# Performance work log

Hardware: AMD Instinct MI355X
Metric: run time of the kernel (lower is better)

Reference implementation:

```python
import jax, jax.numpy as jnp
import numpy as np

B, C, H, W = 8, 512, 64, 64
CQ = C // 8


def conv1x1(x, w, b):
    # x: [B,C,H,W], w: [O,C], b: [O] -> [B,O,H,W]
    return jnp.einsum('bchw,oc->bohw', x, w) + b[None, :, None, None]


def setup_inputs() -> dict:
    key = jax.random.key(0)
    ks = jax.random.split(key, 9)
    sc = 0.05
    return {
        'x2': jax.random.normal(ks[0], (B, C, H, W), jnp.float32),
        'x1': jax.random.normal(ks[1], (B, C, H, W), jnp.float32),
        'q_w': jax.random.normal(ks[2], (CQ, C), jnp.float32) * sc,
        'q_b': jax.random.normal(ks[3], (CQ,), jnp.float32) * sc,
        'k_w': jax.random.normal(ks[4], (CQ, C), jnp.float32) * sc,
        'k_b': jax.random.normal(ks[5], (CQ,), jnp.float32) * sc,
        'v_w': jax.random.normal(ks[6], (C, C), jnp.float32) * sc,
        'v_b': jax.random.normal(ks[7], (C,), jnp.float32) * sc,
        'gamma': jax.random.normal(ks[8], (1,), jnp.float32) * sc,
    }


def reference(x2, x1, q_w, q_b, k_w, k_b, v_w, v_b, gamma):
    h = x2.shape[2]
    q = conv1x1(x2, q_w, q_b)   # [B,CQ,H,W]
    k = conv1x1(x2, k_w, k_b)   # [B,CQ,H,W]
    v2 = conv1x1(x2, v_w, v_b)  # [B,C,H,W]
    v1 = conv1x1(x1, v_w, v_b)  # [B,C,H,W]

    # column (H) attention scores: query at (h,w) vs keys in same column
    energy_H = jnp.einsum('bchw,bcHw->bhwH', q, k)   # [B,H,W,H]
    # row (W) attention scores: query at (h,w) vs keys in same row
    energy_W = jnp.einsum('bchw,bchW->bhwW', q, k)   # [B,H,W,W]
    # NOTE: this module variant does NOT add the diagonal -inf mask.
    concate = jax.nn.softmax(jnp.concatenate([energy_H, energy_W], axis=3), axis=3)
    att_H = concate[..., :h]    # [B,H,W,H]
    att_W = concate[..., h:]    # [B,H,W,W]

    out_H2 = jnp.einsum('bcHw,bhwH->bchw', v2, att_H)
    out_W2 = jnp.einsum('bchW,bhwW->bchw', v2, att_W)
    out_H1 = jnp.einsum('bcHw,bhwH->bchw', v1, att_H)
    out_W1 = jnp.einsum('bchW,bhwW->bchw', v1, att_W)

    g = gamma[0]
    y2 = g * (out_H2 + out_W2) + x2
    y1 = g * (out_H1 + out_W1) + x1
    return (y2, y1)
```

## Files before the change

### kernel.cpp

```cpp
#include <hip/hip_runtime.h>
#include <cstdint>
#include <cstddef>

using u16 = unsigned short;
using u32 = unsigned int;

#define DI __device__ __forceinline__

typedef __attribute__((ext_vector_type(8))) short bf16x8;
typedef __attribute__((ext_vector_type(4))) float f32x4;

DI float bfu2f(u16 u) { return __uint_as_float(((u32)u) << 16); }
DI u16 f2bu(float f) {
    u32 x = __float_as_uint(f);
    return (u16)((x + 0x7fffu + ((x >> 16) & 1u)) >> 16);
}
DI u32 pk2(float a, float b) { return (u32)f2bu(a) | ((u32)f2bu(b) << 16); }

constexpr int CIN = 512;
constexpr int HW  = 4096;
constexpr size_t PLANE = 16777216ull;

__global__ __launch_bounds__(256) void proj_mfma(
    const float* __restrict__ x2, const float* __restrict__ x1,
    const float* __restrict__ q_w, const float* __restrict__ q_b,
    const float* __restrict__ k_w, const float* __restrict__ k_b,
    const float* __restrict__ v_w, const float* __restrict__ v_b,
    u16* __restrict__ oq, u16* __restrict__ ok,
    u16* __restrict__ ov2, u16* __restrict__ ov1)
{
    __shared__ u16 Wlds[128][40];
    __shared__ u16 Xlds[128][40];
    const int tid = threadIdx.x;
    const int m0  = blockIdx.y * 128;
    const int n0g = blockIdx.x * 128;
    const int b    = n0g >> 12;
    const int col0 = n0g & 4095;
    const float* Xb = ((m0 < 640) ? x2 : x1) + (size_t)b * CIN * HW;

    const bool isX = tid < 128;
    const int sr = tid & 127;
    const int mrow = m0 + sr;
    const float* wr;
    if (mrow < 64)        wr = q_w + (size_t)mrow * CIN;
    else if (mrow < 128)  wr = k_w + (size_t)(mrow - 64) * CIN;
    else if (mrow < 640)  wr = v_w + (size_t)(mrow - 128) * CIN;
    else                  wr = v_w + (size_t)(mrow - 640) * CIN;

    const int lane = tid & 63, wv = tid >> 6;
    const int wn = (wv & 1) * 64;
    const int wm = (wv >> 1) * 64;
    const int lr = lane & 15, lq = lane >> 4;

    f32x4 acc[4][4] = {};
    for (int kt = 0; kt < CIN; kt += 32) {
        if (isX) {
            const float* px = Xb + (size_t)kt * HW + col0 + sr;
            u32 pkv[16];
            #pragma unroll
            for (int kk = 0; kk < 16; kk++) {
                float a = px[(size_t)(2 * kk) * HW];
                float c = px[(size_t)(2 * kk + 1) * HW];
                pkv[kk] = pk2(a, c);
            }
            *(uint4*)&Xlds[sr][0]  = *(uint4*)&pkv[0];
            *(uint4*)&Xlds[sr][8]  = *(uint4*)&pkv[4];
            *(uint4*)&Xlds[sr][16] = *(uint4*)&pkv[8];
            *(uint4*)&Xlds[sr][24] = *(uint4*)&pkv[12];
        } else {
            const float* p = wr + kt;
            u32 pw[16];
            #pragma unroll
            for (int t = 0; t < 8; t++) {
                float4 f = *(const float4*)(p + 4 * t);
                pw[2 * t]     = pk2(f.x, f.y);
                pw[2 * t + 1] = pk2(f.z, f.w);
            }
            *(uint4*)&Wlds[sr][0]  = *(uint4*)&pw[0];
            *(uint4*)&Wlds[sr][8]  = *(uint4*)&pw[4];
            *(uint4*)&Wlds[sr][16] = *(uint4*)&pw[8];
            *(uint4*)&Wlds[sr][24] = *(uint4*)&pw[12];
        }
        __syncthreads();
        bf16x8 a[4], bb[4];
        #pragma unroll
        for (int i = 0; i < 4; i++)
            a[i] = *(const bf16x8*)&Xlds[wn + i * 16 + lr][lq * 8];
        #pragma unroll
        for (int j = 0; j < 4; j++)
            bb[j] = *(const bf16x8*)&Wlds[wm + j * 16 + lr][lq * 8];
        #pragma unroll
        for (int j = 0; j < 4; j++)
            #pragma unroll
            for (int i = 0; i < 4; i++)
                acc[i][j] = __builtin_amdgcn_mfma_f32_16x16x32_bf16(a[i], bb[j], acc[i][j], 0, 0, 0);
        __syncthreads();
    }
    #pragma unroll
    for (int j = 0; j < 4; j++) {
        const int mbase = m0 + wm + j * 16;
        const float* bp; u16* op; int ch0, cc;
        if (mbase < 64)       { bp = q_b; op = oq;  ch0 = mbase;       cc = 64;  }
        else if (mbase < 128) { bp = k_b; op = ok;  ch0 = mbase - 64;  cc = 64;  }
        else if (mbase < 640) { bp = v_b; op = ov2; ch0 = mbase - 128; cc = 512; }
        else                  { bp = v_b; op = ov1; ch0 = mbase - 640; cc = 512; }
        const int ch = ch0 + lr;
        const float bias = bp[ch];
        u16* obase = op + ((size_t)b * cc + ch) * HW + col0 + wn + lq * 4;
        #pragma unroll
        for (int i = 0; i < 4; i++) {
            uint2 pkd = { pk2(acc[i][j][0] + bias, acc[i][j][1] + bias),
                          pk2(acc[i][j][2] + bias, acc[i][j][3] + bias) };
            *(uint2*)(obase + i * 16) = pkd;
        }
    }
}

__global__ __launch_bounds__(256) void transpose64_bb(
    const u16* __restrict__ src, u16* __restrict__ dst)
{
    __shared__ u16 t[64][65];
    const size_t s = blockIdx.x;
    const u16* sp = src + s * 4096;
    u16* dp = dst + s * 4096;
    const int tid = threadIdx.x;
    #pragma unroll
    for (int i = 0; i < 16; i++) { int idx = tid + 256 * i; t[idx >> 6][idx & 63] = sp[idx]; }
    __syncthreads();
    #pragma unroll
    for (int i = 0; i < 16; i++) { int idx = tid + 256 * i; dp[idx] = t[idx & 63][idx >> 6]; }
}

__global__ __launch_bounds__(256) void transpose64_bb_inplace(u16* __restrict__ d)
{
    __shared__ u16 t[64][65];
    u16* p = d + (size_t)blockIdx.x * 4096;
    const int tid = threadIdx.x;
    #pragma unroll
    for (int i = 0; i < 16; i++) { int idx = tid + 256 * i; t[idx >> 6][idx & 63] = p[idx]; }
    __syncthreads();
    #pragma unroll
    for (int i = 0; i < 16; i++) { int idx = tid + 256 * i; p[idx] = t[idx & 63][idx >> 6]; }
}

__global__ __launch_bounds__(256) void transpose_cl(
    const u16* __restrict__ src, u16* __restrict__ dst)
{
    __shared__ u16 t[64][65];
    const int s = blockIdx.x;
    const int batch = s >> 6, tile = s & 63;
    const u16* sp = src + (size_t)batch * 262144 + (size_t)tile * 64;
    u16* dp = dst + (size_t)batch * 262144 + (size_t)tile * 4096;
    const int tid = threadIdx.x;
    {
        const int c = tid >> 2, x0 = (tid & 3) * 16;
        *(uint4*)&t[c][x0]     = *(const uint4*)(sp + (size_t)c * 4096 + x0);
        *(uint4*)&t[c][x0 + 8] = *(const uint4*)(sp + (size_t)c * 4096 + x0 + 8);
    }
    __syncthreads();
    {
        const int x = tid >> 2, c0 = (tid & 3) * 16;
        u16 tmp[16];
        #pragma unroll
        for (int i = 0; i < 16; i++) tmp[i] = t[c0 + i][x];
        *(uint4*)&dp[(size_t)x * 64 + c0]     = *(uint4*)&tmp[0];
        *(uint4*)&dp[(size_t)x * 64 + c0 + 8] = *(uint4*)&tmp[8];
    }
}

__global__ __launch_bounds__(256) void energy_h_mfma(
    const u16* __restrict__ qc, const u16* __restrict__ kc, float* __restrict__ e)
{
    __shared__ u16 Qs[64][72], Ks[64][72];
    const int w = blockIdx.x, b = blockIdx.y;
    const int tid = threadIdx.x;
    {
        const int row = tid >> 2, ch = (tid & 3) * 16;
        const size_t g = ((size_t)b * 4096 + (size_t)row * 64 + w) * 64 + ch;
        *(uint4*)&Qs[row][ch]     = *(const uint4*)(qc + g);
        *(uint4*)&Qs[row][ch + 8] = *(const uint4*)(qc + g + 8);
        *(uint4*)&Ks[row][ch]     = *(const uint4*)(kc + g);
        *(uint4*)&Ks[row][ch + 8] = *(const uint4*)(kc + g + 8);
    }
    __syncthreads();
    const int lane = tid & 63, wv = tid >> 6;
    const int mH = (wv & 1) * 32, nh = (wv >> 1) * 32;
    const int lr = lane & 15, lq = lane >> 4;
    f32x4 acc[2][2] = {};
    #pragma unroll
    for (int kt = 0; kt < 2; kt++) {
        const int k0 = kt * 32 + lq * 8;
        bf16x8 afr[2], bfr[2];
        #pragma unroll
        for (int i = 0; i < 2; i++) afr[i] = *(const bf16x8*)&Ks[mH + i * 16 + lr][k0];
        #pragma unroll
        for (int j = 0; j < 2; j++) bfr[j] = *(const bf16x8*)&Qs[nh + j * 16 + lr][k0];
        #pragma unroll
        for (int j = 0; j < 2; j++)
            #pragma unroll
            for (int i = 0; i < 2; i++)
                acc[i][j] = __builtin_amdgcn_mfma_f32_16x16x32_bf16(afr[i], bfr[j], acc[i][j], 0, 0, 0);
    }
    #pragma unroll
    for (int i = 0; i < 2; i++)
        #pragma unroll
        for (int j = 0; j < 2; j++) {
            const int h = nh + j * 16 + lr;
            const int Hp = mH + i * 16 + lq * 4;
            float4 v = make_float4(acc[i][j][0], acc[i][j][1], acc[i][j][2], acc[i][j][3]);
            *reinterpret_cast<float4*>(e + ((size_t)(b * 64 + h) * 64 + w) * 128 + Hp) = v;
        }
}

__global__ __launch_bounds__(256) void energy_w_mfma(
    const u16* __restrict__ qc, const u16* __restrict__ kc, float* __restrict__ e)
{
    __shared__ u16 Qs[64][72], Ks[64][72];
    const int h = blockIdx.x, b = blockIdx.y;
    const int tid = threadIdx.x;
    {
        const int row = tid >> 2, ch = (tid & 3) * 16;
        const size_t g = ((size_t)b * 4096 + (size_t)h * 64 + row) * 64 + ch;
        *(uint4*)&Qs[row][ch]     = *(const uint4*)(qc + g);
        *(uint4*)&Qs[row][ch + 8] = *(const uint4*)(qc + g + 8);
        *(uint4*)&Ks[row][ch]     = *(const uint4*)(kc + g);
        *(uint4*)&Ks[row][ch + 8] = *(const uint4*)(kc + g + 8);
    }
    __syncthreads();
    const int lane = tid & 63, wv = tid >> 6;
    const int mW = (wv & 1) * 32, nw = (wv >> 1) * 32;
    const int lr = lane & 15, lq = lane >> 4;
    f32x4 acc[2][2] = {};
    #pragma unroll
    for (int kt = 0; kt < 2; kt++) {
        const int k0 = kt * 32 + lq * 8;
        bf16x8 afr[2], bfr[2];
        #pragma unroll
        for (int i = 0; i < 2; i++) afr[i] = *(const bf16x8*)&Ks[mW + i * 16 + lr][k0];
        #pragma unroll
        for (int j = 0; j < 2; j++) bfr[j] = *(const bf16x8*)&Qs[nw + j * 16 + lr][k0];
        #pragma unroll
        for (int j = 0; j < 2; j++)
            #pragma unroll
            for (int i = 0; i < 2; i++)
                acc[i][j] = __builtin_amdgcn_mfma_f32_16x16x32_bf16(afr[i], bfr[j], acc[i][j], 0, 0, 0);
    }
    #pragma unroll
    for (int i = 0; i < 2; i++)
        #pragma unroll
        for (int j = 0; j < 2; j++) {
            const int w = nw + j * 16 + lr;
            const int Wp = mW + i * 16 + lq * 4;
            float4 v = make_float4(acc[i][j][0], acc[i][j][1], acc[i][j][2], acc[i][j][3]);
            *reinterpret_cast<float4*>(e + ((size_t)(b * 64 + h) * 64 + w) * 128 + 64 + Wp) = v;
        }
}

__global__ __launch_bounds__(256) void softmax128_bf(
    const float* __restrict__ e, u16* __restrict__ attb)
{
    const int pos = blockIdx.x * 4 + (threadIdx.x >> 6);
    const int l = threadIdx.x & 63;
    const float* p = e + (size_t)pos * 128;
    float v0 = p[l], v1 = p[l + 64];
    float m = fmaxf(v0, v1);
    #pragma unroll
    for (int o = 32; o > 0; o >>= 1) m = fmaxf(m, __shfl_xor(m, o, 64));
    float e0 = __expf(v0 - m), e1 = __expf(v1 - m);
    float s = e0 + e1;
    #pragma unroll
    for (int o = 32; o > 0; o >>= 1) s += __shfl_xor(s, o, 64);
    float inv = 1.0f / s;
    u16* q = attb + (size_t)pos * 128;
    q[l] = f2bu(e0 * inv);
    q[l + 64] = f2bu(e1 * inv);
}

__global__ __launch_bounds__(256) void agg_h_mfma(
    const u16* __restrict__ vTa, const u16* __restrict__ vTb,
    const u16* __restrict__ attb, u16* __restrict__ Pa, u16* __restrict__ Pb)
{
    __shared__ u16 Vs[128][72];
    __shared__ u16 As[64][72];
    const int mt = blockIdx.x, w = blockIdx.y, b = blockIdx.z;
    const u16* vT = (mt < 4) ? vTa : vTb;
    u16*       P  = (mt < 4) ? Pa  : Pb;
    const int c0 = (mt & 3) * 128;
    const int tid = threadIdx.x;
    const u16* va = vT + ((size_t)(b * 512 + c0) * 64 + w) * 64;
    const u16* ab = attb + ((size_t)b * 4096 + w) * 128;
    {
        const int r = tid >> 3, cB = (tid & 7) * 8;
        #pragma unroll
        for (int i = 0; i < 4; i++)
            *(uint4*)&Vs[r + 32 * i][cB] = *(const uint4*)(va + (size_t)(r + 32 * i) * 4096 + cB);
        #pragma unroll
        for (int i = 0; i < 2; i++)
            *(uint4*)&As[r + 32 * i][cB] = *(const uint4*)(ab + (size_t)(r + 32 * i) * 8192 + cB);
    }
    __syncthreads();
    const int lane = tid & 63, wv = tid >> 6;
    const int wm = (wv & 1) * 64, wn = (wv >> 1) * 32;
    const int lr = lane & 15, lq = lane >> 4;
    f32x4 acc[4][2] = {};
    #pragma unroll
    for (int kt = 0; kt < 2; kt++) {
        const int k0 = kt * 32 + lq * 8;
        bf16x8 afr[4], bfr[2];
        #pragma unroll
        for (int i = 0; i < 4; i++) afr[i] = *(const bf16x8*)&Vs[wm + i * 16 + lr][k0];
        #pragma unroll
        for (int j = 0; j < 2; j++) bfr[j] = *(const bf16x8*)&As[wn + j * 16 + lr][k0];
        #pragma unroll
        for (int j = 0; j < 2; j++)
            #pragma unroll
            for (int i = 0; i < 4; i++)
                acc[i][j] = __builtin_amdgcn_mfma_f32_16x16x32_bf16(afr[i], bfr[j], acc[i][j], 0, 0, 0);
    }
    #pragma unroll
    for (int i = 0; i < 4; i++)
        #pragma unroll
        for (int j = 0; j < 2; j++) {
            u16* pp = P + ((size_t)(b * 512 + c0 + wm + i * 16 + lq * 4) * 64 + w) * 64 + wn + j * 16 + lr;
            #pragma unroll
            for (int r = 0; r < 4; r++) pp[(size_t)r * 4096] = f2bu(acc[i][j][r]);
        }
}

__global__ __launch_bounds__(256) void agg_w_mfma(
    const u16* __restrict__ v2, const u16* __restrict__ v1,
    const u16* __restrict__ P2, const u16* __restrict__ P1,
    const u16* __restrict__ attb,
    const float* __restrict__ x2, const float* __restrict__ x1,
    const float* __restrict__ gptr, float* __restrict__ out)
{
    __shared__ u16 Vs[128][72];
    __shared__ u16 As[64][72];
    const int mt = blockIdx.x, h = blockIdx.y, b = blockIdx.z;
    const u16* v = (mt < 4) ? v2 : v1;
    const u16* P = (mt < 4) ? P2 : P1;
    const float* x = (mt < 4) ? x2 : x1;
    float* y = out + ((mt < 4) ? 0 : PLANE);
    const int c0 = (mt & 3) * 128;
    const int tid = threadIdx.x;
    const u16* vb = v + (size_t)(b * 512 + c0) * 4096 + h * 64;
    const u16* ab = attb + ((size_t)(b * 64 + h) * 64) * 128 + 64;
    {
        const int r = tid >> 3, cB = (tid & 7) * 8;
        #pragma unroll
        for (int i = 0; i < 4; i++)
            *(uint4*)&Vs[r + 32 * i][cB] = *(const uint4*)(vb + (size_t)(r + 32 * i) * 4096 + cB);
        #pragma unroll
        for (int i = 0; i < 2; i++)
            *(uint4*)&As[r + 32 * i][cB] = *(const uint4*)(ab + (size_t)(r + 32 * i) * 128 + cB);
    }
    __syncthreads();
    const int lane = tid & 63, wv = tid >> 6;
    const int wm = (wv & 1) * 64, wn = (wv >> 1) * 32;
    const int lr = lane & 15, lq = lane >> 4;
    f32x4 acc[4][2] = {};
    #pragma unroll
    for (int kt = 0; kt < 2; kt++) {
        const int k0 = kt * 32 + lq * 8;
        bf16x8 afr[4], bfr[2];
        #pragma unroll
        for (int i = 0; i < 4; i++) afr[i] = *(const bf16x8*)&Vs[wm + i * 16 + lr][k0];
        #pragma unroll
        for (int j = 0; j < 2; j++) bfr[j] = *(const bf16x8*)&As[wn + j * 16 + lr][k0];
        #pragma unroll
        for (int j = 0; j < 2; j++)
            #pragma unroll
            for (int i = 0; i < 4; i++)
                acc[i][j] = __builtin_amdgcn_mfma_f32_16x16x32_bf16(afr[i], bfr[j], acc[i][j], 0, 0, 0);
    }
    const float g = gptr[0];
    #pragma unroll
    for (int i = 0; i < 4; i++)
        #pragma unroll
        for (int j = 0; j < 2; j++) {
            size_t off = (size_t)(b * 512 + c0 + wm + i * 16 + lq * 4) * 4096
                       + (size_t)h * 64 + wn + j * 16 + lr;
            #pragma unroll
            for (int r = 0; r < 4; r++) {
                size_t o = off + (size_t)r * 4096;
                y[o] = g * (bfu2f(P[o]) + acc[i][j][r]) + x[o];
            }
        }
}

extern "C" void kernel_launch(void* const* d_in, const int* in_sizes, int n_in,
                              void* d_out, int out_size, void* d_ws, size_t ws_size,
                              hipStream_t stream)
{
    (void)in_sizes; (void)n_in; (void)out_size; (void)ws_size;
    const float* x2  = (const float*)d_in[0];
    const float* x1  = (const float*)d_in[1];
    const float* q_w = (const float*)d_in[2];
    const float* q_b = (const float*)d_in[3];
    const float* k_w = (const float*)d_in[4];
    const float* k_b = (const float*)d_in[5];
    const float* v_w = (const float*)d_in[6];
    const float* v_b = (const float*)d_in[7];
    const float* gm  = (const float*)d_in[8];

    char* ws = (char*)d_ws;
    u16*   v2   = (u16*)(ws);
    u16*   v1   = (u16*)(ws + ((size_t)32  << 20));
    u16*   attb = (u16*)(ws + ((size_t)64  << 20));
    u16*   q    = (u16*)(ws + ((size_t)72  << 20));
    u16*   k    = (u16*)(ws + ((size_t)76  << 20));
    u16*   qc   = (u16*)(ws + ((size_t)80  << 20));
    u16*   kc   = (u16*)(ws + ((size_t)84  << 20));
    float* e    = (float*)(ws + ((size_t)88 << 20));
    u16*   vT2  = (u16*)(ws + ((size_t)72  << 20));
    u16*   vT1  = (u16*)(ws + ((size_t)104 << 20));
    float* out = (float*)d_out;

    dim3 blk(256);
    proj_mfma<<<dim3(256, 9), blk, 0, stream>>>(x2, x1, q_w, q_b, k_w, k_b,
                                                v_w, v_b, q, k, v2, v1);
    transpose_cl<<<1024, blk, 0, stream>>>(q, qc);
    energy_h_mfma<<<dim3(64, 8), blk, 0, stream>>>(qc, kc, e);
    energy_w_mfma<<<dim3(64, 8), blk, 0, stream>>>(qc, kc, e);
    softmax128_bf<<<8192, blk, 0, stream>>>(e, attb);
    transpose64_bb<<<8192, blk, 0, stream>>>(v2, vT2);
    agg_h_mfma<<<dim3(8, 64, 8), blk, 0, stream>>>(vT2, vT1, attb, vT2, vT1);
    transpose64_bb_inplace<<<8192, blk, 0, stream>>>(vT2);
    agg_w_mfma<<<dim3(8, 64, 8), blk, 0, stream>>>(v2, v1, vT2, vT1, attb,
                                                   x2, x1, gm, out);
}
```

Measured before the change: 499.3 us.

## Pre-convert inputs and weights to bf16 channel-last before projection GEMM

Adds two prep kernels: one packs q/k/v weights into a single bf16 matrix, the other transposes x2/x1 into bf16 channel-last layout. The projection GEMM can then load contiguous 16-byte rows instead of strided fp32 column reads with per-element conversion, and its K-tile grows from 32 to 64. The cost is an extra full read/write pass over both inputs, more workspace, and two more launches. The workspace offsets are reshuffled so XT buffers alias regions that later kernels reuse.

```diff
diff --git a/kernel.cpp b/kernel.cpp
--- a/kernel.cpp
+++ b/kernel.cpp
@@ -21,31 +21,76 @@
 constexpr int HW  = 4096;
 constexpr size_t PLANE = 16777216ull;
 
+__global__ __launch_bounds__(256) void wcat_bf16(
+    const float* __restrict__ q_w, const float* __restrict__ k_w,
+    const float* __restrict__ v_w, u16* __restrict__ Wcat)
+{
+    const int gid = blockIdx.x * 256 + threadIdx.x;
+    const int e0 = gid * 8;
+    const int row = e0 >> 9, col = e0 & 511;
+    const float* src = (row < 64)  ? q_w + ((size_t)row << 9)
+                     : (row < 128) ? k_w + ((size_t)(row - 64) << 9)
+                                   : v_w + ((size_t)(row - 128) << 9);
+    float4 f0 = *(const float4*)(src + col), f1 = *(const float4*)(src + col + 4);
+    uint4 u = { pk2(f0.x, f0.y), pk2(f0.z, f0.w), pk2(f1.x, f1.y), pk2(f1.z, f1.w) };
+    *(uint4*)(Wcat + e0) = u;
+}
+
+__global__ __launch_bounds__(256) void x_cl_bf16(
+    const float* __restrict__ x2, const float* __restrict__ x1,
+    u16* __restrict__ XT2, u16* __restrict__ XT1)
+{
+    __shared__ u16 t[64][72];
+    const int st = blockIdx.x;
+    const int ct = blockIdx.y & 7, sel = blockIdx.y >> 3;
+    const int b  = blockIdx.z;
+    const float* x = sel ? x1 : x2;
+    u16* XT = sel ? XT1 : XT2;
+    const int tid = threadIdx.x;
+    const int c0 = ct * 64, s0 = st * 64;
+    {
+        const int c = tid >> 2, q = (tid & 3) * 16;
+        const float* p = x + ((size_t)b * 512 + c0 + c) * 4096 + s0 + q;
+        float4 f0 = *(const float4*)p,       f1 = *(const float4*)(p + 4);
+        float4 f2 = *(const float4*)(p + 8), f3 = *(const float4*)(p + 12);
+        uint4 u0 = { pk2(f0.x, f0.y), pk2(f0.z, f0.w), pk2(f1.x, f1.y), pk2(f1.z, f1.w) };
+        uint4 u1 = { pk2(f2.x, f2.y), pk2(f2.z, f2.w), pk2(f3.x, f3.y), pk2(f3.z, f3.w) };
+        *(uint4*)&t[c][q]     = u0;
+        *(uint4*)&t[c][q + 8] = u1;
+    }
+    __syncthreads();
+    {
+        const int s = tid >> 2, q = (tid & 3) * 16;
+        u16 tmp[16];
+        #pragma unroll
+        for (int i = 0; i < 16; i++) tmp[i] = t[q + i][s];
+        u16* dp = XT + ((size_t)b * 4096 + s0 + s) * 512 + c0 + q;
+        *(uint4*)&dp[0] = *(uint4*)&tmp[0];
+        *(uint4*)&dp[8] = *(uint4*)&tmp[8];
+    }
+}
+
 __global__ __launch_bounds__(256) void proj_mfma(
-    const float* __restrict__ x2, const float* __restrict__ x1,
-    const float* __restrict__ q_w, const float* __restrict__ q_b,
-    const float* __restrict__ k_w, const float* __restrict__ k_b,
-    const float* __restrict__ v_w, const float* __restrict__ v_b,
+    const u16* __restrict__ XT2, const u16* __restrict__ XT1,
+    const u16* __restrict__ Wcat,
+    const float* __restrict__ q_b, const float* __restrict__ k_b,
+    const float* __restrict__ v_b,
     u16* __restrict__ oq, u16* __restrict__ ok,
     u16* __restrict__ ov2, u16* __restrict__ ov1)
 {
-    __shared__ u16 Wlds[128][40];
-    __shared__ u16 Xlds[128][40];
+    __shared__ u16 Xl[128][72];
+    __shared__ u16 Wl[128][72];
     const int tid = threadIdx.x;
     const int m0  = blockIdx.y * 128;
     const int n0g = blockIdx.x * 128;
     const int b    = n0g >> 12;
     const int col0 = n0g & 4095;
-    const float* Xb = ((m0 < 640) ? x2 : x1) + (size_t)b * CIN * HW;
-
-    const bool isX = tid < 128;
-    const int sr = tid & 127;
-    const int mrow = m0 + sr;
-    const float* wr;
-    if (mrow < 64)        wr = q_w + (size_t)mrow * CIN;
-    else if (mrow < 128)  wr = k_w + (size_t)(mrow - 64) * CIN;
-    else if (mrow < 640)  wr = v_w + (size_t)(mrow - 128) * CIN;
-    else                  wr = v_w + (size_t)(mrow - 640) * CIN;
+    const u16* Xb = ((m0 < 640) ? XT2 : XT1) + ((size_t)b * 4096 + col0) * 512;
+    const u16* Wb = Wcat + (size_t)((m0 < 640) ? m0 : m0 - 512) * 512;
+
+    const int srow = tid >> 1, soff = (tid & 1) * 32;
+    const u16* xp = Xb + (size_t)srow * 512 + soff;
+    const u16* wp = Wb + (size_t)srow * 512 + soff;
 
     const int lane = tid & 63, wv = tid >> 6;
     const int wn = (wv & 1) * 64;
@@ -53,47 +98,29 @@
     const int lr = lane & 15, lq = lane >> 4;
 
     f32x4 acc[4][4] = {};
-    for (int kt = 0; kt < CIN; kt += 32) {
-        if (isX) {
-            const float* px = Xb + (size_t)kt * HW + col0 + sr;
-            u32 pkv[16];
-            #pragma unroll
-            for (int kk = 0; kk < 16; kk++) {
-                float a = px[(size_t)(2 * kk) * HW];
-                float c = px[(size_t)(2 * kk + 1) * HW];
-                pkv[kk] = pk2(a, c);
-            }
-            *(uint4*)&Xlds[sr][0]  = *(uint4*)&pkv[0];
-            *(uint4*)&Xlds[sr][8]  = *(uint4*)&pkv[4];
-            *(uint4*)&Xlds[sr][16] = *(uint4*)&pkv[8];
-            *(uint4*)&Xlds[sr][24] = *(uint4*)&pkv[12];
-        } else {
-            const float* p = wr + kt;
-            u32 pw[16];
-            #pragma unroll
-            for (int t = 0; t < 8; t++) {
-                float4 f = *(const float4*)(p + 4 * t);
-                pw[2 * t]     = pk2(f.x, f.y);
-                pw[2 * t + 1] = pk2(f.z, f.w);
-            }
-            *(uint4*)&Wlds[sr][0]  = *(uint4*)&pw[0];
-            *(uint4*)&Wlds[sr][8]  = *(uint4*)&pw[4];
-            *(uint4*)&Wlds[sr][16] = *(uint4*)&pw[8];
-            *(uint4*)&Wlds[sr][24] = *(uint4*)&pw[12];
+    for (int kt = 0; kt < CIN; kt += 64) {
+        #pragma unroll
+        for (int t = 0; t < 4; t++) {
+            *(uint4*)&Xl[srow][soff + 8 * t] = *(const uint4*)(xp + kt + 8 * t);
+            *(uint4*)&Wl[srow][soff + 8 * t] = *(const uint4*)(wp + kt + 8 * t);
         }
         __syncthreads();
-        bf16x8 a[4], bb[4];
-        #pragma unroll
-        for (int i = 0; i < 4; i++)
-            a[i] = *(const bf16x8*)&Xlds[wn + i * 16 + lr][lq * 8];
-        #pragma unroll
-        for (int j = 0; j < 4; j++)
-            bb[j] = *(const bf16x8*)&Wlds[wm + j * 16 + lr][lq * 8];
-        #pragma unroll
-        for (int j = 0; j < 4; j++)
+        #pragma unroll
+        for (int ks = 0; ks < 2; ks++) {
+            const int k0 = ks * 32 + lq * 8;
+            bf16x8 a[4], bb[4];
             #pragma unroll
             for (int i = 0; i < 4; i++)
-                acc[i][j] = __builtin_amdgcn_mfma_f32_16x16x32_bf16(a[i], bb[j], acc[i][j], 0, 0, 0);
+                a[i] = *(const bf16x8*)&Xl[wn + i * 16 + lr][k0];
+            #pragma unroll
+            for (int j = 0; j < 4; j++)
+                bb[j] = *(const bf16x8*)&Wl[wm + j * 16 + lr][k0];
+            #pragma unroll
+            for (int j = 0; j < 4; j++)
+                #pragma unroll
+                for (int i = 0; i < 4; i++)
+                    acc[i][j] = __builtin_amdgcn_mfma_f32_16x16x32_bf16(a[i], bb[j], acc[i][j], 0, 0, 0);
+        }
         __syncthreads();
     }
     #pragma unroll
@@ -407,18 +434,23 @@
     u16*   v2   = (u16*)(ws);
     u16*   v1   = (u16*)(ws + ((size_t)32  << 20));
     u16*   attb = (u16*)(ws + ((size_t)64  << 20));
-    u16*   q    = (u16*)(ws + ((size_t)72  << 20));
-    u16*   k    = (u16*)(ws + ((size_t)76  << 20));
+    u16*   XT2  = (u16*)(ws + ((size_t)64  << 20));
+    u16*   XT1  = (u16*)(ws + ((size_t)96  << 20));
+    u16*   Wcat = (u16*)(ws + ((size_t)128 << 20));
     u16*   qc   = (u16*)(ws + ((size_t)80  << 20));
     u16*   kc   = (u16*)(ws + ((size_t)84  << 20));
     float* e    = (float*)(ws + ((size_t)88 << 20));
     u16*   vT2  = (u16*)(ws + ((size_t)72  << 20));
     u16*   vT1  = (u16*)(ws + ((size_t)104 << 20));
+    u16*   q    = (u16*)(ws + ((size_t)136 << 20));
+    u16*   k    = (u16*)(ws + ((size_t)140 << 20));
     float* out = (float*)d_out;
 
     dim3 blk(256);
-    proj_mfma<<<dim3(256, 9), blk, 0, stream>>>(x2, x1, q_w, q_b, k_w, k_b,
-                                                v_w, v_b, q, k, v2, v1);
+    wcat_bf16<<<160, blk, 0, stream>>>(q_w, k_w, v_w, Wcat);
+    x_cl_bf16<<<dim3(64, 16, 8), blk, 0, stream>>>(x2, x1, XT2, XT1);
+    proj_mfma<<<dim3(256, 9), blk, 0, stream>>>(XT2, XT1, Wcat, q_b, k_b, v_b,
+                                                q, k, v2, v1);
     transpose_cl<<<1024, blk, 0, stream>>>(q, qc);
     energy_h_mfma<<<dim3(64, 8), blk, 0, stream>>>(qc, kc, e);
     energy_w_mfma<<<dim3(64, 8), blk, 0, stream>>>(qc, kc, e);
```

Measured after the change: 472.5 us. -5.4%, faster.
